# Performance work log

Measured on AMD Instinct MI355X. Metric: run time of the kernel, lower is better.

## Reference

```python
import jax, jax.numpy as jnp
import numpy as np

B, T, D, H = 4, 1024, 1024, 16
DH = D // H
EPS = 1e-5


def setup_inputs() -> dict:
    key = jax.random.key(0)
    ks = jax.random.split(key, 14)
    sc = 1.0 / np.sqrt(D)
    x = jax.random.normal(ks[0], (B, T, D), jnp.float32)
    W_r = jax.random.normal(ks[1], (D, D), jnp.float32) * sc
    W_k = jax.random.normal(ks[2], (D, D), jnp.float32) * sc
    W_v = jax.random.normal(ks[3], (D, D), jnp.float32) * sc
    W_w = jax.random.normal(ks[4], (D, D), jnp.float32) * sc
    W_o = jax.random.normal(ks[5], (D, D), jnp.float32) * sc
    u = jax.random.normal(ks[6], (H, DH), jnp.float32) * 0.1
    tm_r = jax.random.uniform(ks[7], (D,), jnp.float32)
    tm_k = jax.random.uniform(ks[8], (D,), jnp.float32)
    tm_v = jax.random.uniform(ks[9], (D,), jnp.float32)
    tm_w = jax.random.uniform(ks[10], (D,), jnp.float32)
    ln_w = jnp.ones((DH,), jnp.float32) + 0.1 * jax.random.normal(ks[11], (DH,), jnp.float32)
    ln_b = 0.1 * jax.random.normal(ks[12], (DH,), jnp.float32)
    return {"x": x, "W_r": W_r, "W_k": W_k, "W_v": W_v, "W_w": W_w, "W_o": W_o,
            "u": u, "tm_r": tm_r, "tm_k": tm_k, "tm_v": tm_v, "tm_w": tm_w,
            "ln_w": ln_w, "ln_b": ln_b}


def _rwkv6(x, W_r, W_k, W_v, W_w, W_o, u, tm_r, tm_k, tm_v, tm_w, ln_w, ln_b):
    b, t, d = x.shape
    # token-shift mix
    x_prev = jnp.concatenate([jnp.zeros_like(x[:, :1]), x[:, :-1]], axis=1)
    xr = tm_r * x + (1.0 - tm_r) * x_prev
    xk = tm_k * x + (1.0 - tm_k) * x_prev
    xv = tm_v * x + (1.0 - tm_v) * x_prev
    xw = tm_w * x + (1.0 - tm_w) * x_prev
    r = jax.nn.sigmoid(xr @ W_r.T)          # (B,T,D)
    k = xk @ W_k.T
    v = xv @ W_v.T
    w = -jax.nn.softplus(-(xw @ W_w.T)) - 1e-4  # always < 0 -> exp(w) in (0,1)
    r = r.reshape(b, t, H, DH)
    k = k.reshape(b, t, H, DH)
    v = v.reshape(b, t, H, DH)
    w = w.reshape(b, t, H, DH)

    def step(s, rkvw):
        r_t, k_t, v_t, w_t = rkvw  # each (B,H,DH)
        bonus = jnp.exp(u + k_t)[..., :, None] * v_t[..., None, :]  # (B,H,DH,DH)
        o_t = jnp.einsum('bhi,bhij->bhj', r_t, s + bonus)
        s = jnp.exp(w_t)[..., None] * s + k_t[..., :, None] * v_t[..., None, :]
        return s, o_t

    s0 = jnp.zeros((b, H, DH, DH), x.dtype)
    rkvw = tuple(a.transpose(1, 0, 2, 3) for a in (r, k, v, w))  # (T,B,H,DH)
    _, o = jax.lax.scan(step, s0, rkvw)      # o: (T,B,H,DH)
    o = o.transpose(1, 0, 2, 3)              # (B,T,H,DH)
    # group LayerNorm over head dim
    mu = jnp.mean(o, axis=-1, keepdims=True)
    var = jnp.var(o, axis=-1, keepdims=True)
    o = (o - mu) * jax.lax.rsqrt(var + EPS) * ln_w + ln_b
    o = o * r
    return (o.reshape(b, t, d)) @ W_o.T


def reference(x, W_r, W_k, W_v, W_w, W_o, u, tm_r, tm_k, tm_v, tm_w, ln_w, ln_b):
    return _rwkv6(x, W_r, W_k, W_v, W_w, W_o, u, tm_r, tm_k, tm_v, tm_w, ln_w, ln_b)
```

## Files before the change

kernel.cpp:

```cpp
#include <hip/hip_runtime.h>


typedef unsigned short u16;
typedef unsigned int   u32;

typedef __attribute__((ext_vector_type(8))) __bf16 bf16x8;
typedef __attribute__((ext_vector_type(4))) float   f32x4;

#define MB (1u << 20)

#define LDS_PTR(p) ((__attribute__((address_space(3))) void*)(p))
#define GLB_PTR(p) ((const __attribute__((address_space(1))) void*)(p))

__device__ __forceinline__ u16 f2bf(float f) {
  u32 u = __builtin_bit_cast(u32, f);
  u += 0x7FFFu + ((u >> 16) & 1u);
  return (u16)(u >> 16);
}
__device__ __forceinline__ float bf2f(u16 x) {
  u32 u = ((u32)x) << 16;
  return __builtin_bit_cast(float, u);
}
__device__ __forceinline__ u32 pack2(float a, float b) {
  return (u32)f2bf(a) | ((u32)f2bf(b) << 16);
}

__global__ __launch_bounds__(256) void prep_w(
    const float* __restrict__ w0, const float* __restrict__ w1,
    const float* __restrict__ w2, const float* __restrict__ w3,
    const float* __restrict__ w4, u32* __restrict__ out) {
  int idx = blockIdx.x * 256 + threadIdx.x;
  int m = idx >> 19;
  int l = idx & 524287;
  const float* src = (m == 0) ? w0 : (m == 1) ? w1 : (m == 2) ? w2 : (m == 3) ? w3 : w4;
  float2 v = *(const float2*)(src + (size_t)l * 2);
  out[idx] = pack2(v.x, v.y);
}

__global__ __launch_bounds__(256) void prep_mix(
    const float* __restrict__ x,
    const float* __restrict__ tmr, const float* __restrict__ tmk,
    const float* __restrict__ tmv, const float* __restrict__ tmw,
    u32* __restrict__ xr, u32* __restrict__ xk,
    u32* __restrict__ xv, u32* __restrict__ xw) {
  int idx = blockIdx.x * 256 + threadIdx.x;
  int t  = (idx >> 9) & 1023;
  int d0 = (idx & 511) * 2;
  size_t e = (size_t)idx * 2;
  float2 xc = *(const float2*)(x + e);
  float2 xp = make_float2(0.f, 0.f);
  if (t > 0) xp = *(const float2*)(x + e - 1024);
  float2 tm;
  tm = *(const float2*)(tmr + d0);
  xr[idx] = pack2(tm.x * xc.x + (1.f - tm.x) * xp.x, tm.y * xc.y + (1.f - tm.y) * xp.y);
  tm = *(const float2*)(tmk + d0);
  xk[idx] = pack2(tm.x * xc.x + (1.f - tm.x) * xp.x, tm.y * xc.y + (1.f - tm.y) * xp.y);
  tm = *(const float2*)(tmv + d0);
  xv[idx] = pack2(tm.x * xc.x + (1.f - tm.x) * xp.x, tm.y * xc.y + (1.f - tm.y) * xp.y);
  tm = *(const float2*)(tmw + d0);
  xw[idx] = pack2(tm.x * xc.x + (1.f - tm.x) * xp.x, tm.y * xc.y + (1.f - tm.y) * xp.y);
}

__global__ __launch_bounds__(512, 1) void gemm_proj(
    const u16* __restrict__ xr, const u16* __restrict__ xk,
    const u16* __restrict__ xv, const u16* __restrict__ xw,
    const u16* __restrict__ Wr, const u16* __restrict__ Wk,
    const u16* __restrict__ Wv, const u16* __restrict__ Ww,
    u16* __restrict__ rO, u16* __restrict__ kO,
    u16* __restrict__ vO, float* __restrict__ wO) {
  constexpr int KITER = 16;
  constexpr int LDK   = 1024;
  __shared__ __align__(16) u16 Asm[2 * 16384];
  __shared__ __align__(16) u16 Bsm[2 * 16384];

  int mat = blockIdx.z;
  const u16* A = (mat == 0) ? xr : (mat == 1) ? xk : (mat == 2) ? xv : xw;
  const u16* W = (mat == 0) ? Wr : (mat == 1) ? Wk : (mat == 2) ? Wv : Ww;

  int tid = threadIdx.x;
  int m0 = blockIdx.x * 256, n0 = blockIdx.y * 256;
  int wave = tid >> 6, lane = tid & 63;
  int wm = (wave >> 2) * 128;
  int wn = (wave & 3) * 64;
  int r16 = lane & 15, quad = lane >> 4;

  f32x4 acc[8][4] = {};

  int lrow  = lane >> 3;
  int lchk  = (lane & 7) ^ lrow;
  const u16* Ag[4];
  const u16* Bg[4];
#pragma unroll
  for (int i = 0; i < 4; ++i) {
    int row = wave * 32 + i * 8 + lrow;
    Ag[i] = A + (size_t)(m0 + row) * LDK + lchk * 8;
    Bg[i] = W + (size_t)(n0 + row) * LDK + lchk * 8;
  }
  int ldsW = wave * 2048;

  int aoff[8], boff[4];
#pragma unroll
  for (int mt = 0; mt < 8; ++mt) {
    int r = wm + mt * 16 + r16;
    aoff[mt] = r * 64 + (quad ^ (r16 & 7)) * 8;
  }
#pragma unroll
  for (int nt = 0; nt < 4; ++nt) {
    int r = wn + nt * 16 + r16;
    boff[nt] = r * 64 + (quad ^ (r16 & 7)) * 8;
  }

#define ISSUE_TILE(t, buf)                                                              \
  do {                                                                                  \
    int _o = (buf) * 16384 + ldsW, _k = (t) * 64;                                       \
    __builtin_amdgcn_global_load_lds(GLB_PTR(Ag[0] + _k), LDS_PTR(Asm + _o),        16, 0, 0); \
    __builtin_amdgcn_global_load_lds(GLB_PTR(Ag[1] + _k), LDS_PTR(Asm + _o + 512),  16, 0, 0); \
    __builtin_amdgcn_global_load_lds(GLB_PTR(Ag[2] + _k), LDS_PTR(Asm + _o + 1024), 16, 0, 0); \
    __builtin_amdgcn_global_load_lds(GLB_PTR(Ag[3] + _k), LDS_PTR(Asm + _o + 1536), 16, 0, 0); \
    __builtin_amdgcn_global_load_lds(GLB_PTR(Bg[0] + _k), LDS_PTR(Bsm + _o),        16, 0, 0); \
    __builtin_amdgcn_global_load_lds(GLB_PTR(Bg[1] + _k), LDS_PTR(Bsm + _o + 512),  16, 0, 0); \
    __builtin_amdgcn_global_load_lds(GLB_PTR(Bg[2] + _k), LDS_PTR(Bsm + _o + 1024), 16, 0, 0); \
    __builtin_amdgcn_global_load_lds(GLB_PTR(Bg[3] + _k), LDS_PTR(Bsm + _o + 1536), 16, 0, 0); \
  } while (0)

  ISSUE_TILE(0, 0);
  ISSUE_TILE(1, 1);

  int cur = 0;
  for (int i = 0; i < KITER; ++i) {
    if (i < KITER - 1) asm volatile("s_waitcnt vmcnt(8)" ::: "memory");
    else               asm volatile("s_waitcnt vmcnt(0)" ::: "memory");
    __builtin_amdgcn_s_barrier();

    const u16* As = Asm + cur * 16384;
    const u16* Bs = Bsm + cur * 16384;
#pragma unroll
    for (int kk = 0; kk < 2; ++kk) {
      int kx = kk * 32;
      bf16x8 af[8], bfm[4];
#pragma unroll
      for (int mt = 0; mt < 8; ++mt) af[mt] = *(const bf16x8*)&As[aoff[mt] ^ kx];
#pragma unroll
      for (int nt = 0; nt < 4; ++nt) bfm[nt] = *(const bf16x8*)&Bs[boff[nt] ^ kx];
#pragma unroll
      for (int mt = 0; mt < 8; ++mt)
#pragma unroll
        for (int nt = 0; nt < 4; ++nt)
          acc[mt][nt] = __builtin_amdgcn_mfma_f32_16x16x32_bf16(af[mt], bfm[nt], acc[mt][nt], 0, 0, 0);
    }

    asm volatile("s_waitcnt lgkmcnt(0)" ::: "memory");
    __builtin_amdgcn_s_barrier();
    if (i + 2 < KITER) ISSUE_TILE(i + 2, cur);
    cur ^= 1;
  }
#undef ISSUE_TILE

#pragma unroll
  for (int mt = 0; mt < 8; ++mt) {
#pragma unroll
    for (int nt = 0; nt < 4; ++nt) {
#pragma unroll
      for (int rg = 0; rg < 4; ++rg) {
        int row = m0 + wm + mt * 16 + quad * 4 + rg;
        int col = n0 + wn + nt * 16 + r16;
        float v = acc[mt][nt][rg];
        size_t idx = (size_t)row * 1024 + col;
        if (mat == 0)      rO[idx] = f2bf(1.f / (1.f + __expf(-v)));
        else if (mat == 1) kO[idx] = f2bf(v);
        else if (mat == 2) vO[idx] = f2bf(v);
        else               wO[idx] = v;
      }
    }
  }
}

__global__ __launch_bounds__(512, 1) void gemm_out_sk(
    const u16* __restrict__ A, const u16* __restrict__ W,
    float* __restrict__ O) {
  constexpr int KITER = 8;
  constexpr int LDK   = 1024;
  __shared__ __align__(16) u16 SMEM[2][2][2][8192];

  int tid = threadIdx.x;
  int m0 = blockIdx.x * 128, n0 = blockIdx.y * 128;
  int wave = tid >> 6, lane = tid & 63;
  int grp = wave >> 2, w4 = wave & 3;
  int wm = (w4 >> 1) * 64, wn = (w4 & 1) * 64;
  int r16 = lane & 15, quad = lane >> 4;

  f32x4 acc[4][4] = {};

  int lrow  = lane >> 3;
  int lchk  = (lane & 7) ^ lrow;
  const u16* Ag[4];
  const u16* Bg[4];
#pragma unroll
  for (int i = 0; i < 4; ++i) {
    int row = w4 * 32 + i * 8 + lrow;
    Ag[i] = A + (size_t)(m0 + row) * LDK + grp * 512 + lchk * 8;
    Bg[i] = W + (size_t)(n0 + row) * LDK + grp * 512 + lchk * 8;
  }
  u16* Abase = &SMEM[0][grp][0][0];
  u16* Bbase = &SMEM[1][grp][0][0];
  int ldsW = w4 * 2048;

  int aoff[4], boff[4];
#pragma unroll
  for (int mt = 0; mt < 4; ++mt) {
    int r = wm + mt * 16 + r16;
    aoff[mt] = r * 64 + (quad ^ (r16 & 7)) * 8;
  }
#pragma unroll
  for (int nt = 0; nt < 4; ++nt) {
    int r = wn + nt * 16 + r16;
    boff[nt] = r * 64 + (quad ^ (r16 & 7)) * 8;
  }

#define ISSUE_TILE(t, buf)                                                              \
  do {                                                                                  \
    int _o = (buf) * 8192 + ldsW, _k = (t) * 64;                                        \
    __builtin_amdgcn_global_load_lds(GLB_PTR(Ag[0] + _k), LDS_PTR(Abase + _o),        16, 0, 0); \
    __builtin_amdgcn_global_load_lds(GLB_PTR(Ag[1] + _k), LDS_PTR(Abase + _o + 512),  16, 0, 0); \
    __builtin_amdgcn_global_load_lds(GLB_PTR(Ag[2] + _k), LDS_PTR(Abase + _o + 1024), 16, 0, 0); \
    __builtin_amdgcn_global_load_lds(GLB_PTR(Ag[3] + _k), LDS_PTR(Abase + _o + 1536), 16, 0, 0); \
    __builtin_amdgcn_global_load_lds(GLB_PTR(Bg[0] + _k), LDS_PTR(Bbase + _o),        16, 0, 0); \
    __builtin_amdgcn_global_load_lds(GLB_PTR(Bg[1] + _k), LDS_PTR(Bbase + _o + 512),  16, 0, 0); \
    __builtin_amdgcn_global_load_lds(GLB_PTR(Bg[2] + _k), LDS_PTR(Bbase + _o + 1024), 16, 0, 0); \
    __builtin_amdgcn_global_load_lds(GLB_PTR(Bg[3] + _k), LDS_PTR(Bbase + _o + 1536), 16, 0, 0); \
  } while (0)

  ISSUE_TILE(0, 0);
  ISSUE_TILE(1, 1);

  int cur = 0;
  for (int i = 0; i < KITER; ++i) {
    if (i < KITER - 1) asm volatile("s_waitcnt vmcnt(8)" ::: "memory");
    else               asm volatile("s_waitcnt vmcnt(0)" ::: "memory");
    __builtin_amdgcn_s_barrier();

    const u16* As = Abase + cur * 8192;
    const u16* Bs = Bbase + cur * 8192;
#pragma unroll
    for (int kk = 0; kk < 2; ++kk) {
      int kx = kk * 32;
      bf16x8 af[4], bfm[4];
#pragma unroll
      for (int mt = 0; mt < 4; ++mt) af[mt] = *(const bf16x8*)&As[aoff[mt] ^ kx];
#pragma unroll
      for (int nt = 0; nt < 4; ++nt) bfm[nt] = *(const bf16x8*)&Bs[boff[nt] ^ kx];
#pragma unroll
      for (int mt = 0; mt < 4; ++mt)
#pragma unroll
        for (int nt = 0; nt < 4; ++nt)
          acc[mt][nt] = __builtin_amdgcn_mfma_f32_16x16x32_bf16(af[mt], bfm[nt], acc[mt][nt], 0, 0, 0);
    }

    asm volatile("s_waitcnt lgkmcnt(0)" ::: "memory");
    __builtin_amdgcn_s_barrier();
    if (i + 2 < KITER) ISSUE_TILE(i + 2, cur);
    cur ^= 1;
  }
#undef ISSUE_TILE

  float* red = (float*)&SMEM[0][0][0][0];
  int slot = (tid & 255) * 68;
  if (grp == 1) {
#pragma unroll
    for (int mt = 0; mt < 4; ++mt)
#pragma unroll
      for (int nt = 0; nt < 4; ++nt)
        *(f32x4*)&red[slot + (mt * 4 + nt) * 4] = acc[mt][nt];
  }
  __syncthreads();
  if (grp == 0) {
#pragma unroll
    for (int mt = 0; mt < 4; ++mt) {
#pragma unroll
      for (int nt = 0; nt < 4; ++nt) {
        f32x4 other = *(const f32x4*)&red[slot + (mt * 4 + nt) * 4];
#pragma unroll
        for (int rg = 0; rg < 4; ++rg) {
          int row = m0 + wm + mt * 16 + quad * 4 + rg;
          int col = n0 + wn + nt * 16 + r16;
          O[(size_t)row * 1024 + col] = acc[mt][nt][rg] + other[rg];
        }
      }
    }
  }
}

__global__ __launch_bounds__(256) void scan_intra(
    const u16* __restrict__ rb, const u16* __restrict__ kb,
    const u16* __restrict__ vb, const float* __restrict__ wb,
    const float* __restrict__ u,
    float* __restrict__ o, u16* __restrict__ rd,
    float* __restrict__ U, float* __restrict__ Dc) {
  int c = blockIdx.x, bh = blockIdx.y;
  int b = bh >> 4, h = bh & 15;
  int tid = threadIdx.x;
  int wave = tid >> 6, lane = tid & 63;
  int ig4 = tid >> 4, jq = tid & 15;

  __shared__ __align__(16) float4 combo[4][64];
  __shared__ __align__(16) float4 vs4[4][16];
  __shared__ __align__(16) float  part[4][16][68];

  const float EW_SCALE = 0.99990001f;

  float s[4][4];
#pragma unroll
  for (int ii = 0; ii < 4; ++ii)
#pragma unroll
    for (int jj = 0; jj < 4; ++jj) s[ii][jj] = 0.f;

  size_t base = ((size_t)(b * 1024 + c * 32)) * 1024 + h * 64 + lane;
  float dloc = 1.0f;
  float uval = (wave < 2) ? u[h * 64 + lane] : 0.f;

#define STAGE(t2, sl)                                                     \
  do {                                                                    \
    size_t _idx = base + (size_t)(t2) * 1024;                             \
    if (wave < 2) {                                                       \
      float _r = bf2f(rb[_idx]);                                          \
      float _k = bf2f(kb[_idx]);                                          \
      float _z = wb[_idx];                                                \
      combo[sl][lane] = make_float4(_r, _k, __expf(uval + _k),            \
                                    EW_SCALE / (1.f + __expf(-_z)));      \
    } else {                                                              \
      ((float*)vs4)[(sl) * 64 + lane] = bf2f(vb[_idx]);                   \
    }                                                                     \
  } while (0)

  { int p = wave & 1; STAGE(p, p); }
  __syncthreads();

  for (int tt = 0; tt < 32; tt += 2) {
    if (tt + 2 < 32) {
      int p = wave & 1;
      int t2 = tt + 2 + p;
      STAGE(t2, t2 & 3);
    }
#pragma unroll
    for (int p = 0; p < 2; ++p) {
      int t = tt + p, sl = t & 3;
      float4 vv = vs4[sl][jq];
      float4 cb0 = combo[sl][ig4 * 4 + 0];
      float4 cb1 = combo[sl][ig4 * 4 + 1];
      float4 cb2 = combo[sl][ig4 * 4 + 2];
      float4 cb3 = combo[sl][ig4 * 4 + 3];
      float ac0 = 0.f, ac1 = 0.f, ac2 = 0.f, ac3 = 0.f;
#define ROW(cb, ii)                                                       \
      do {                                                                \
        float t0 = fmaf(cb.z, vv.x, s[ii][0]);                            \
        float t1 = fmaf(cb.z, vv.y, s[ii][1]);                            \
        float t2_ = fmaf(cb.z, vv.z, s[ii][2]);                           \
        float t3 = fmaf(cb.z, vv.w, s[ii][3]);                            \
        ac0 = fmaf(cb.x, t0, ac0);                                        \
        ac1 = fmaf(cb.x, t1, ac1);                                        \
        ac2 = fmaf(cb.x, t2_, ac2);                                       \
        ac3 = fmaf(cb.x, t3, ac3);                                        \
        s[ii][0] = fmaf(cb.w, s[ii][0], cb.y * vv.x);                     \
        s[ii][1] = fmaf(cb.w, s[ii][1], cb.y * vv.y);                     \
        s[ii][2] = fmaf(cb.w, s[ii][2], cb.y * vv.z);                     \
        s[ii][3] = fmaf(cb.w, s[ii][3], cb.y * vv.w);                     \
      } while (0)
      ROW(cb0, 0); ROW(cb1, 1); ROW(cb2, 2); ROW(cb3, 3);
#undef ROW
      *(float4*)&part[sl][ig4][jq * 4] = make_float4(ac0, ac1, ac2, ac3);
      if (wave == 0) {
        float4 me = combo[sl][lane];
        rd[base + (size_t)t * 1024] = f2bf(me.x * dloc);
        dloc *= me.w;
      }
    }
    if (tt >= 2) {
      if (wave == 2) {
        int t = tt - 2, sl = t & 3;
        float sum = 0.f;
#pragma unroll
        for (int g = 0; g < 16; ++g) sum += part[sl][g][lane];
        o[base + (size_t)t * 1024] = sum;
      } else if (wave == 3) {
        int t = tt - 1, sl = t & 3;
        float sum = 0.f;
#pragma unroll
        for (int g = 0; g < 16; ++g) sum += part[sl][g][lane];
        o[base + (size_t)t * 1024] = sum;
      }
    }
    __syncthreads();
  }
#undef STAGE
  if (wave == 2) {
    float sum = 0.f;
#pragma unroll
    for (int g = 0; g < 16; ++g) sum += part[2][g][lane];
    o[base + (size_t)30 * 1024] = sum;
  } else if (wave == 3) {
    float sum = 0.f;
#pragma unroll
    for (int g = 0; g < 16; ++g) sum += part[3][g][lane];
    o[base + (size_t)31 * 1024] = sum;
  }

  float* Ug = U + (size_t)(bh * 32 + c) * 4096;
#pragma unroll
  for (int ii = 0; ii < 4; ++ii) {
    *(float4*)&Ug[(ig4 * 4 + ii) * 64 + jq * 4] =
        make_float4(s[ii][0], s[ii][1], s[ii][2], s[ii][3]);
  }
  if (wave == 0) Dc[(bh * 32 + c) * 64 + lane] = dloc;
}

__global__ __launch_bounds__(256) void state_prop(
    float* __restrict__ U, const float* __restrict__ Dc) {
  int bh  = blockIdx.x >> 4;
  int e   = (blockIdx.x & 15) * 256 + threadIdx.x;
  int i   = e >> 6;
  float acc = 0.f;
  for (int c = 0; c < 32; ++c) {
    float* Ug = U + (size_t)(bh * 32 + c) * 4096 + e;
    float d = Dc[(bh * 32 + c) * 64 + i];
    float uv = *Ug;
    *Ug = acc;
    acc = fmaf(d, acc, uv);
  }
}

__global__ __launch_bounds__(128) void inter_ln(
    const float* __restrict__ o, const u16* __restrict__ rd,
    const u16* __restrict__ rb, const float* __restrict__ U,
    const float* __restrict__ lnw, const float* __restrict__ lnb,
    u16* __restrict__ oh) {
  int c = blockIdx.x, bh = blockIdx.y;
  int b = bh >> 4, h = bh & 15;
  int tid = threadIdx.x, wave = tid >> 6, lane = tid & 63;
  int l15 = lane & 15, quad = lane >> 4;

  __shared__ __align__(16) u16 Sb[64][72];

  const float* Sg = U + (size_t)(bh * 32 + c) * 4096;
#pragma unroll
  for (int q = 0; q < 32; ++q) {
    int e = q * 128 + tid;
    Sb[e & 63][e >> 6] = f2bf(Sg[e]);
  }
  __syncthreads();

  size_t rbase = ((size_t)(b * 1024 + c * 32)) * 1024 + h * 64;

  const u16* rdg = rd + rbase + (size_t)(wave * 16 + l15) * 1024 + quad * 8;
  bf16x8 af0 = *(const bf16x8*)(rdg);
  bf16x8 af1 = *(const bf16x8*)(rdg + 32);

  f32x4 acc[4] = {};
#pragma unroll
  for (int nt = 0; nt < 4; ++nt) {
    const u16* bp = &Sb[nt * 16 + l15][quad * 8];
    bf16x8 b0 = *(const bf16x8*)bp;
    bf16x8 b1 = *(const bf16x8*)(bp + 32);
    acc[nt] = __builtin_amdgcn_mfma_f32_16x16x32_bf16(af0, b0, acc[nt], 0, 0, 0);
    acc[nt] = __builtin_amdgcn_mfma_f32_16x16x32_bf16(af1, b1, acc[nt], 0, 0, 0);
  }

#pragma unroll
  for (int rg = 0; rg < 4; ++rg) {
    int t = wave * 16 + quad * 4 + rg;
    size_t rowb = rbase + (size_t)t * 1024;
    float v[4];
    float s1 = 0.f, s2 = 0.f;
#pragma unroll
    for (int nt = 0; nt < 4; ++nt) {
      v[nt] = acc[nt][rg] + o[rowb + nt * 16 + l15];
      s1 += v[nt];
      s2 += v[nt] * v[nt];
    }
#pragma unroll
    for (int m = 1; m < 16; m <<= 1) {
      s1 += __shfl_xor(s1, m, 64);
      s2 += __shfl_xor(s2, m, 64);
    }
    float mu  = s1 * (1.f / 64.f);
    float var = s2 * (1.f / 64.f) - mu * mu;
    float rstd = rsqrtf(var + 1e-5f);
#pragma unroll
    for (int nt = 0; nt < 4; ++nt) {
      int jj = nt * 16 + l15;
      float nv = (v[nt] - mu) * rstd;
      float val = (nv * lnw[jj] + lnb[jj]) * bf2f(rb[rowb + jj]);
      oh[rowb + jj] = f2bf(val);
    }
  }
}

extern "C" void kernel_launch(void* const* d_in, const int* in_sizes, int n_in,
                              void* d_out, int out_size, void* d_ws, size_t ws_size,
                              hipStream_t stream) {
  const float* x    = (const float*)d_in[0];
  const float* W_r  = (const float*)d_in[1];
  const float* W_k  = (const float*)d_in[2];
  const float* W_v  = (const float*)d_in[3];
  const float* W_w  = (const float*)d_in[4];
  const float* W_o  = (const float*)d_in[5];
  const float* u    = (const float*)d_in[6];
  const float* tm_r = (const float*)d_in[7];
  const float* tm_k = (const float*)d_in[8];
  const float* tm_v = (const float*)d_in[9];
  const float* tm_w = (const float*)d_in[10];
  const float* ln_w = (const float*)d_in[11];
  const float* ln_b = (const float*)d_in[12];
  float* out = (float*)d_out;

  char* ws = (char*)d_ws;
  u16* xr = (u16*)(ws + (size_t)0 * MB);
  u16* xk = (u16*)(ws + (size_t)8 * MB);
  u16* xv = (u16*)(ws + (size_t)16 * MB);
  u16* xw = (u16*)(ws + (size_t)24 * MB);
  float* Ubuf = (float*)(ws + (size_t)0 * MB);
  u16* Wb = (u16*)(ws + (size_t)32 * MB);
  u16* Wrb = Wb;
  u16* Wkb = (u16*)(ws + (size_t)34 * MB);
  u16* Wvb = (u16*)(ws + (size_t)36 * MB);
  u16* Wwb = (u16*)(ws + (size_t)38 * MB);
  u16* Wob = (u16*)(ws + (size_t)40 * MB);
  float* Dcbuf = (float*)(ws + (size_t)42 * MB);
  u16*   rbuf = (u16*)(ws + (size_t)48 * MB);
  u16*   kbuf = (u16*)(ws + (size_t)56 * MB);
  u16*   vbuf = (u16*)(ws + (size_t)64 * MB);
  float* wbuf = (float*)(ws + (size_t)72 * MB);
  float* obuf = (float*)(ws + (size_t)88 * MB);
  u16*  rdbuf = (u16*)(ws + (size_t)104 * MB);
  u16*   ohbuf = (u16*)(ws + (size_t)129 * MB);

  prep_w<<<10240, 256, 0, stream>>>(W_r, W_k, W_v, W_w, W_o, (u32*)Wb);
  prep_mix<<<8192, 256, 0, stream>>>(x, tm_r, tm_k, tm_v, tm_w,
                                     (u32*)xr, (u32*)xk, (u32*)xv, (u32*)xw);
  gemm_proj<<<dim3(16, 4, 4), 512, 0, stream>>>(xr, xk, xv, xw,
                                                Wrb, Wkb, Wvb, Wwb,
                                                rbuf, kbuf, vbuf, wbuf);
  scan_intra<<<dim3(32, 64), 256, 0, stream>>>(rbuf, kbuf, vbuf, wbuf, u,
                                               obuf, rdbuf, Ubuf, Dcbuf);
  state_prop<<<1024, 256, 0, stream>>>(Ubuf, Dcbuf);
  inter_ln<<<dim3(32, 64), 128, 0, stream>>>(obuf, rdbuf, rbuf, Ubuf,
                                             ln_w, ln_b, ohbuf);
  gemm_out_sk<<<dim3(32, 8), 512, 0, stream>>>(ohbuf, Wob, out);
}
```

Baseline: 238.8 us.

## Merge prep kernels, remap GEMM block order for XCD locality, store scan state as bf16

The weight conversion and token-shift mix kernels are merged into one launch, removing a kernel launch and its gap. Both GEMMs now use a 1D grid with a custom block-index remap, so blocks sharing A or B tiles land on the same XCD under round-robin dispatch, which should improve L2 reuse. state_prop now writes the propagated state as bf16 into a separate buffer (reusing the w region), instead of rewriting fp32 in place. This halves the state traffic read by inter_ln and drops its conversion, at the cost of aliasing a buffer that must already be dead.

```diff
diff --git a/kernel.cpp b/kernel.cpp
--- a/kernel.cpp
+++ b/kernel.cpp
@@ -25,40 +25,41 @@
   return (u32)f2bf(a) | ((u32)f2bf(b) << 16);
 }
 
-__global__ __launch_bounds__(256) void prep_w(
+__global__ __launch_bounds__(256) void prep_all(
     const float* __restrict__ w0, const float* __restrict__ w1,
     const float* __restrict__ w2, const float* __restrict__ w3,
-    const float* __restrict__ w4, u32* __restrict__ out) {
-  int idx = blockIdx.x * 256 + threadIdx.x;
-  int m = idx >> 19;
-  int l = idx & 524287;
-  const float* src = (m == 0) ? w0 : (m == 1) ? w1 : (m == 2) ? w2 : (m == 3) ? w3 : w4;
-  float2 v = *(const float2*)(src + (size_t)l * 2);
-  out[idx] = pack2(v.x, v.y);
-}
-
-__global__ __launch_bounds__(256) void prep_mix(
+    const float* __restrict__ w4, u32* __restrict__ wout,
     const float* __restrict__ x,
     const float* __restrict__ tmr, const float* __restrict__ tmk,
     const float* __restrict__ tmv, const float* __restrict__ tmw,
     u32* __restrict__ xr, u32* __restrict__ xk,
     u32* __restrict__ xv, u32* __restrict__ xw) {
-  int idx = blockIdx.x * 256 + threadIdx.x;
-  int t  = (idx >> 9) & 1023;
-  int d0 = (idx & 511) * 2;
-  size_t e = (size_t)idx * 2;
-  float2 xc = *(const float2*)(x + e);
-  float2 xp = make_float2(0.f, 0.f);
-  if (t > 0) xp = *(const float2*)(x + e - 1024);
-  float2 tm;
-  tm = *(const float2*)(tmr + d0);
-  xr[idx] = pack2(tm.x * xc.x + (1.f - tm.x) * xp.x, tm.y * xc.y + (1.f - tm.y) * xp.y);
-  tm = *(const float2*)(tmk + d0);
-  xk[idx] = pack2(tm.x * xc.x + (1.f - tm.x) * xp.x, tm.y * xc.y + (1.f - tm.y) * xp.y);
-  tm = *(const float2*)(tmv + d0);
-  xv[idx] = pack2(tm.x * xc.x + (1.f - tm.x) * xp.x, tm.y * xc.y + (1.f - tm.y) * xp.y);
-  tm = *(const float2*)(tmw + d0);
-  xw[idx] = pack2(tm.x * xc.x + (1.f - tm.x) * xp.x, tm.y * xc.y + (1.f - tm.y) * xp.y);
+  int bid = blockIdx.x;
+  if (bid < 10240) {
+    int idx = bid * 256 + threadIdx.x;
+    int m = idx >> 19;
+    int l = idx & 524287;
+    const float* src = (m == 0) ? w0 : (m == 1) ? w1 : (m == 2) ? w2 : (m == 3) ? w3 : w4;
+    float2 v = *(const float2*)(src + (size_t)l * 2);
+    wout[idx] = pack2(v.x, v.y);
+  } else {
+    int idx = (bid - 10240) * 256 + threadIdx.x;
+    int t  = (idx >> 9) & 1023;
+    int d0 = (idx & 511) * 2;
+    size_t e = (size_t)idx * 2;
+    float2 xc = *(const float2*)(x + e);
+    float2 xp = make_float2(0.f, 0.f);
+    if (t > 0) xp = *(const float2*)(x + e - 1024);
+    float2 tm;
+    tm = *(const float2*)(tmr + d0);
+    xr[idx] = pack2(tm.x * xc.x + (1.f - tm.x) * xp.x, tm.y * xc.y + (1.f - tm.y) * xp.y);
+    tm = *(const float2*)(tmk + d0);
+    xk[idx] = pack2(tm.x * xc.x + (1.f - tm.x) * xp.x, tm.y * xc.y + (1.f - tm.y) * xp.y);
+    tm = *(const float2*)(tmv + d0);
+    xv[idx] = pack2(tm.x * xc.x + (1.f - tm.x) * xp.x, tm.y * xc.y + (1.f - tm.y) * xp.y);
+    tm = *(const float2*)(tmw + d0);
+    xw[idx] = pack2(tm.x * xc.x + (1.f - tm.x) * xp.x, tm.y * xc.y + (1.f - tm.y) * xp.y);
+  }
 }
 
 __global__ __launch_bounds__(512, 1) void gemm_proj(
@@ -73,12 +74,18 @@
   __shared__ __align__(16) u16 Asm[2 * 16384];
   __shared__ __align__(16) u16 Bsm[2 * 16384];
 
-  int mat = blockIdx.z;
+  int d  = blockIdx.x;
+  int k8 = d & 7, q = d >> 3;
+  int gh = q >> 4;
+  int xt = q & 15;
+  int g  = k8 + 8 * gh;
+  int yt = g & 3, mat = g >> 2;
+
   const u16* A = (mat == 0) ? xr : (mat == 1) ? xk : (mat == 2) ? xv : xw;
   const u16* W = (mat == 0) ? Wr : (mat == 1) ? Wk : (mat == 2) ? Wv : Ww;
 
   int tid = threadIdx.x;
-  int m0 = blockIdx.x * 256, n0 = blockIdx.y * 256;
+  int m0 = xt * 256, n0 = yt * 256;
   int wave = tid >> 6, lane = tid & 63;
   int wm = (wave >> 2) * 128;
   int wn = (wave & 3) * 64;
@@ -182,8 +189,14 @@
   constexpr int LDK   = 1024;
   __shared__ __align__(16) u16 SMEM[2][2][2][8192];
 
+  int d  = blockIdx.x;
+  int k8 = d & 7, q = d >> 3;
+  int gh = q >> 3;
+  int yt = q & 7;
+  int xt = k8 + 8 * gh;
+
   int tid = threadIdx.x;
-  int m0 = blockIdx.x * 128, n0 = blockIdx.y * 128;
+  int m0 = xt * 128, n0 = yt * 128;
   int wave = tid >> 6, lane = tid & 63;
   int grp = wave >> 2, w4 = wave & 3;
   int wm = (w4 >> 1) * 64, wn = (w4 & 1) * 64;
@@ -414,23 +427,23 @@
 }
 
 __global__ __launch_bounds__(256) void state_prop(
-    float* __restrict__ U, const float* __restrict__ Dc) {
+    const float* __restrict__ U, const float* __restrict__ Dc,
+    u16* __restrict__ ST) {
   int bh  = blockIdx.x >> 4;
   int e   = (blockIdx.x & 15) * 256 + threadIdx.x;
   int i   = e >> 6;
   float acc = 0.f;
   for (int c = 0; c < 32; ++c) {
-    float* Ug = U + (size_t)(bh * 32 + c) * 4096 + e;
-    float d = Dc[(bh * 32 + c) * 64 + i];
-    float uv = *Ug;
-    *Ug = acc;
+    float d  = Dc[(bh * 32 + c) * 64 + i];
+    float uv = U[(size_t)(bh * 32 + c) * 4096 + e];
+    ST[(size_t)(bh * 32 + c) * 4096 + e] = f2bf(acc);
     acc = fmaf(d, acc, uv);
   }
 }
 
 __global__ __launch_bounds__(128) void inter_ln(
     const float* __restrict__ o, const u16* __restrict__ rd,
-    const u16* __restrict__ rb, const float* __restrict__ U,
+    const u16* __restrict__ rb, const u16* __restrict__ ST,
     const float* __restrict__ lnw, const float* __restrict__ lnb,
     u16* __restrict__ oh) {
   int c = blockIdx.x, bh = blockIdx.y;
@@ -440,11 +453,11 @@
 
   __shared__ __align__(16) u16 Sb[64][72];
 
-  const float* Sg = U + (size_t)(bh * 32 + c) * 4096;
+  const u16* Sg = ST + (size_t)(bh * 32 + c) * 4096;
 #pragma unroll
   for (int q = 0; q < 32; ++q) {
     int e = q * 128 + tid;
-    Sb[e & 63][e >> 6] = f2bf(Sg[e]);
+    Sb[e & 63][e >> 6] = Sg[e];
   }
   __syncthreads();
 
@@ -529,20 +542,21 @@
   u16*   kbuf = (u16*)(ws + (size_t)56 * MB);
   u16*   vbuf = (u16*)(ws + (size_t)64 * MB);
   float* wbuf = (float*)(ws + (size_t)72 * MB);
+  u16*   Sbuf = (u16*)(ws + (size_t)72 * MB);
   float* obuf = (float*)(ws + (size_t)88 * MB);
   u16*  rdbuf = (u16*)(ws + (size_t)104 * MB);
   u16*   ohbuf = (u16*)(ws + (size_t)129 * MB);
 
-  prep_w<<<10240, 256, 0, stream>>>(W_r, W_k, W_v, W_w, W_o, (u32*)Wb);
-  prep_mix<<<8192, 256, 0, stream>>>(x, tm_r, tm_k, tm_v, tm_w,
-                                     (u32*)xr, (u32*)xk, (u32*)xv, (u32*)xw);
-  gemm_proj<<<dim3(16, 4, 4), 512, 0, stream>>>(xr, xk, xv, xw,
-                                                Wrb, Wkb, Wvb, Wwb,
-                                                rbuf, kbuf, vbuf, wbuf);
+  prep_all<<<18432, 256, 0, stream>>>(W_r, W_k, W_v, W_w, W_o, (u32*)Wb,
+                                      x, tm_r, tm_k, tm_v, tm_w,
+                                      (u32*)xr, (u32*)xk, (u32*)xv, (u32*)xw);
+  gemm_proj<<<256, 512, 0, stream>>>(xr, xk, xv, xw,
+                                     Wrb, Wkb, Wvb, Wwb,
+                                     rbuf, kbuf, vbuf, wbuf);
   scan_intra<<<dim3(32, 64), 256, 0, stream>>>(rbuf, kbuf, vbuf, wbuf, u,
                                                obuf, rdbuf, Ubuf, Dcbuf);
-  state_prop<<<1024, 256, 0, stream>>>(Ubuf, Dcbuf);
-  inter_ln<<<dim3(32, 64), 128, 0, stream>>>(obuf, rdbuf, rbuf, Ubuf,
+  state_prop<<<1024, 256, 0, stream>>>(Ubuf, Dcbuf, Sbuf);
+  inter_ln<<<dim3(32, 64), 128, 0, stream>>>(obuf, rdbuf, rbuf, Sbuf,
                                              ln_w, ln_b, ohbuf);
-  gemm_out_sk<<<dim3(32, 8), 512, 0, stream>>>(ohbuf, Wob, out);
-}
+  gemm_out_sk<<<256, 512, 0, stream>>>(ohbuf, Wob, out);
+}
```

Measured after the change: 232.8 us. -2.5%, faster.
